# Kernel tuning notes

Hardware: AMD Instinct MI355X
Metric: run time of the kernel (lower is better)

## Reference

```python
import jax, jax.numpy as jnp
import numpy as np

H = 1024   # hidden_size
I = 4096   # intermediate_size
E = 8      # num_local_experts
K = 2      # num_experts_per_tok
B, S = 2, 2048


def setup_inputs() -> dict:
    key = jax.random.key(0)
    ks = jax.random.split(key, 7)
    init = lambda k, shape, fan_in: (jax.random.normal(k, shape, jnp.float32)
                                     / np.float32(np.sqrt(fan_in)))
    return {
        "x": jax.random.normal(ks[0], (B, S, H), jnp.float32),
        "router_gate": init(ks[1], (E, H), H),   # router for gate_proj
        "w_gate": init(ks[2], (E, I, H), H),     # expert weights gate_proj
        "router_up": init(ks[3], (E, H), H),     # router for up_proj
        "w_up": init(ks[4], (E, I, H), H),       # expert weights up_proj
        "router_down": init(ks[5], (E, I), I),   # router for down_proj
        "w_down": init(ks[6], (E, H, I), I),     # expert weights down_proj
    }


def _moe_linear(x, router_w, expert_w):
    """Top-K routed linear. x:[T,din] router_w:[E,din] expert_w:[E,dout,din]."""
    n_exp = router_w.shape[0]
    logits = x @ router_w.T                      # [T, E]
    vals, idx = jax.lax.top_k(logits, K)         # [T, K]
    probs = jax.nn.softmax(vals, axis=-1)        # softmax over selected experts
    onehot = jax.nn.one_hot(idx, n_exp, dtype=x.dtype)    # [T, K, E]
    combine = jnp.einsum('tk,tke->te', probs, onehot)     # [T, E] sparse combine weights
    out = jnp.zeros((x.shape[0], expert_w.shape[1]), x.dtype)
    for e in range(n_exp):  # fixed small expert count
        out = out + combine[:, e:e + 1] * (x @ expert_w[e].T)
    return out


def reference(x, router_gate, w_gate, router_up, w_up, router_down, w_down):
    b, s, h = x.shape
    xt = x.reshape(b * s, h)                     # tokens [T, H]
    g = _moe_linear(xt, router_gate, w_gate)     # [T, I]
    u = _moe_linear(xt, router_up, w_up)         # [T, I]
    inter = jax.nn.silu(g) * u                   # SwiGLU
    d = _moe_linear(inter, router_down, w_down)  # [T, H]
    return d.reshape(b, s, h)
```

## Files before the change

kernel.cpp:

```cpp
#include <hip/hip_runtime.h>
#include <cmath>

typedef float    f32x4 __attribute__((ext_vector_type(4)));
typedef _Float16 f16x8 __attribute__((ext_vector_type(8)));

#define T_NUM 4096
#define H_DIM 1024
#define I_DIM 4096
#define MAXTILES 40

#define M_COUNTS   0
#define M_CURSORS  48
#define M_OFFSETS  96
#define M_NTILES   144
#define M_TILE_E   152
#define M_TILE_M   392
#define M_TOPKI    1024
#define M_TOPKP    25600
#define M_STOK     50176
#define M_SPRB     74752

__device__ __forceinline__ float wave_sum(float v) {
  v += __shfl_xor(v, 32);
  v += __shfl_xor(v, 16);
  v += __shfl_xor(v, 8);
  v += __shfl_xor(v, 4);
  v += __shfl_xor(v, 2);
  v += __shfl_xor(v, 1);
  return v;
}

__device__ __forceinline__ void topk_write(int* meta, int layer, int t, const float* v) {
  int e0 = 0; float v0 = v[0];
  #pragma unroll
  for (int e = 1; e < 8; ++e) { if (v[e] > v0) { v0 = v[e]; e0 = e; } }
  int e1 = 0; float v1 = -3.4e38f;
  #pragma unroll
  for (int e = 0; e < 8; ++e) { if (e != e0 && v[e] > v1) { v1 = v[e]; e1 = e; } }
  float ex = expf(v1 - v0);
  float p0 = 1.f / (1.f + ex);
  float p1 = ex / (1.f + ex);
  meta[M_TOPKI + (layer * T_NUM + t) * 2    ] = e0;
  meta[M_TOPKI + (layer * T_NUM + t) * 2 + 1] = e1;
  ((float*)meta)[M_TOPKP + (layer * T_NUM + t) * 2    ] = p0;
  ((float*)meta)[M_TOPKP + (layer * T_NUM + t) * 2 + 1] = p1;
}

__global__ __launch_bounds__(256) void router_gu(const float* __restrict__ x,
    const float* __restrict__ Rg, const float* __restrict__ Ru, int* __restrict__ meta)
{
  int w = threadIdx.x >> 6, lane = threadIdx.x & 63;
  int t = blockIdx.x * 4 + w;
  const float* xr = x + (size_t)t * H_DIM + lane * 4;
  f32x4 xv[4];
  #pragma unroll
  for (int c = 0; c < 4; ++c) xv[c] = *(const f32x4*)(xr + c * 256);
  float lg[8], lu[8];
  #pragma unroll
  for (int e = 0; e < 8; ++e) {
    const float* rg = Rg + (size_t)e * H_DIM + lane * 4;
    const float* ru = Ru + (size_t)e * H_DIM + lane * 4;
    float sg = 0.f, su = 0.f;
    #pragma unroll
    for (int c = 0; c < 4; ++c) {
      f32x4 a = *(const f32x4*)(rg + c * 256);
      f32x4 b = *(const f32x4*)(ru + c * 256);
      sg += a[0]*xv[c][0] + a[1]*xv[c][1] + a[2]*xv[c][2] + a[3]*xv[c][3];
      su += b[0]*xv[c][0] + b[1]*xv[c][1] + b[2]*xv[c][2] + b[3]*xv[c][3];
    }
    lg[e] = wave_sum(sg);
    lu[e] = wave_sum(su);
  }
  if (lane == 0) {
    topk_write(meta, 0, t, lg);
    topk_write(meta, 1, t, lu);
  }
}

__global__ __launch_bounds__(256) void route_finalize(int* __restrict__ meta, int l0, int nl) {
  __shared__ int cnt_s[32];
  __shared__ int off_s[32];
  __shared__ int cur_s[32];
  int tid = threadIdx.x;
  if (tid < 32) { cnt_s[tid] = 0; cur_s[tid] = 0; }
  __syncthreads();
  for (int t = tid; t < T_NUM; t += 256) {
    for (int l = l0; l < l0 + nl; ++l) {
      int li = l - l0;
      #pragma unroll
      for (int k = 0; k < 2; ++k) {
        int e = meta[M_TOPKI + (l * T_NUM + t) * 2 + k];
        atomicAdd(&cnt_s[li * 16 + k * 8 + e], 1);
      }
    }
  }
  __syncthreads();
  if (tid == 0) {
    for (int l = l0; l < l0 + nl; ++l) {
      int li = l - l0;
      int off = 0;
      for (int k = 0; k < 2; ++k) {
        int nt = 0;
        for (int e = 0; e < 8; ++e) {
          int s = (l * 2 + k) * 8 + e;
          int c = cnt_s[li * 16 + k * 8 + e];
          meta[M_COUNTS + s] = c;
          meta[M_OFFSETS + s] = off;
          off_s[li * 16 + k * 8 + e] = off;
          for (int m = 0; m < c; m += 128) {
            meta[M_TILE_E + (l * 2 + k) * MAXTILES + nt] = e;
            meta[M_TILE_M + (l * 2 + k) * MAXTILES + nt] = m;
            ++nt;
          }
          off += c;
        }
        meta[M_NTILES + l * 2 + k] = nt;
      }
    }
  }
  __syncthreads();
  for (int t = tid; t < T_NUM; t += 256) {
    for (int l = l0; l < l0 + nl; ++l) {
      int li = l - l0;
      #pragma unroll
      for (int k = 0; k < 2; ++k) {
        int e = meta[M_TOPKI + (l * T_NUM + t) * 2 + k];
        float p = ((float*)meta)[M_TOPKP + (l * T_NUM + t) * 2 + k];
        int si = li * 16 + k * 8 + e;
        int pos = off_s[si] + atomicAdd(&cur_s[si], 1);
        meta[M_STOK + l * 8192 + pos] = t;
        ((float*)meta)[M_SPRB + l * 8192 + pos] = p;
      }
    }
  }
}

template<int SPLITS>
__global__ __launch_bounds__(256) void convert_w(const float* __restrict__ W,
    _Float16* __restrict__ Whi, _Float16* __restrict__ Wlo, int NB, int KT)
{
  size_t g = (size_t)blockIdx.x * 256 + threadIdx.x;
  int c   = (int)(g >> 9);
  int rem = (int)(g & 511);
  int fq = rem >> 7, r = rem & 127;
  int e  = c / (NB * KT);
  int nb = (c / KT) % NB;
  int kt = c - (c / KT) * KT;
  int K = KT * 32, N = NB * 128;
  const float* src = W + ((size_t)(e * N + nb * 128 + r)) * K + kt * 32 + fq * 8;
  f32x4 v0 = *(const f32x4*)src;
  f32x4 v1 = *(const f32x4*)(src + 4);
  f16x8 h, l;
  #pragma unroll
  for (int q = 0; q < 8; ++q) {
    float v = (q < 4) ? v0[q] : v1[q - 4];
    _Float16 hv = (_Float16)v;
    h[q] = hv;
    l[q] = (_Float16)(v - (float)hv);
  }
  size_t dst = (size_t)c * 4096 + (size_t)rem * 8;
  *(f16x8*)(Whi + dst) = h;
  if constexpr (SPLITS == 3) *(f16x8*)(Wlo + dst) = l;
}

__global__ __launch_bounds__(256) void gather_a(const float* __restrict__ X,
    _Float16* __restrict__ Apass, const int* __restrict__ meta, int layer, int kk)
{
  int pass = layer * 2 + kk;
  int tile = blockIdx.x >> 5;
  int kt   = blockIdx.x & 31;
  if (tile >= meta[M_NTILES + pass]) return;
  int e    = meta[M_TILE_E + pass * MAXTILES + tile];
  int m0   = meta[M_TILE_M + pass * MAXTILES + tile];
  int sidx = pass * 8 + e;
  int cnt  = meta[M_COUNTS + sidx];
  int seg  = meta[M_OFFSETS + sidx];
  const int* stok = meta + M_STOK + layer * 8192 + seg;
  size_t cb = ((size_t)tile * 32 + kt) * 8192;
  #pragma unroll
  for (int j = 0; j < 2; ++j) {
    int idx = threadIdx.x * 2 + j;
    int fq = idx >> 7, row = idx & 127;
    int m = m0 + row; if (m >= cnt) m = cnt - 1;
    const float* src = X + (size_t)stok[m] * H_DIM + kt * 32 + fq * 8;
    f32x4 v0 = *(const f32x4*)src;
    f32x4 v1 = *(const f32x4*)(src + 4);
    f16x8 h, l;
    #pragma unroll
    for (int q = 0; q < 8; ++q) {
      float v = (q < 4) ? v0[q] : v1[q - 4];
      _Float16 hv = (_Float16)v;
      h[q] = hv;
      l[q] = (_Float16)(v - (float)hv);
    }
    *(f16x8*)(Apass + cb + (size_t)idx * 8) = h;
    *(f16x8*)(Apass + cb + 4096 + (size_t)idx * 8) = l;
  }
}

__global__ __launch_bounds__(256) void gather_d(const float* __restrict__ G,
    _Float16* __restrict__ Ad, const int* __restrict__ meta, int kk)
{
  int pass = 4 + kk;
  int tile = blockIdx.x >> 7;
  int kt   = blockIdx.x & 127;
  if (tile >= meta[M_NTILES + pass]) return;
  int e    = meta[M_TILE_E + pass * MAXTILES + tile];
  int m0   = meta[M_TILE_M + pass * MAXTILES + tile];
  int sidx = pass * 8 + e;
  int cnt  = meta[M_COUNTS + sidx];
  int seg  = meta[M_OFFSETS + sidx];
  const int* stok = meta + M_STOK + 2 * 8192 + seg;
  size_t cb = ((size_t)tile * 128 + kt) * 4096;
  #pragma unroll
  for (int j = 0; j < 2; ++j) {
    int idx = threadIdx.x * 2 + j;
    int fq = idx >> 7, row = idx & 127;
    int m = m0 + row; if (m >= cnt) m = cnt - 1;
    const float* src = G + (size_t)stok[m] * I_DIM + kt * 32 + fq * 8;
    f32x4 v0 = *(const f32x4*)src;
    f32x4 v1 = *(const f32x4*)(src + 4);
    f16x8 h;
    #pragma unroll
    for (int q = 0; q < 8; ++q) h[q] = (_Float16)((q < 4) ? v0[q] : v1[q - 4]);
    *(f16x8*)(Ad + cb + (size_t)idx * 8) = h;
  }
}

__device__ __forceinline__ void gload16(const _Float16* g, _Float16* l) {
  __builtin_amdgcn_global_load_lds(
      (const __attribute__((address_space(1))) void*)g,
      (__attribute__((address_space(3))) void*)l, 16, 0, 0);
}

template<int SPLITS, int ADD, int N, int NB, int STEPS, int SPLITK>
__global__ __launch_bounds__(256, 2) void moe_gemm7(
    const _Float16* __restrict__ Aimg,
    const _Float16* __restrict__ Whi, const _Float16* __restrict__ Wlo,
    float* __restrict__ Out, float* __restrict__ Scr,
    const int* __restrict__ meta, int layer, int kk)
{
  constexpr int NWG = MAXTILES * NB * SPLITK;
  constexpr int Q8  = NWG / 8;
  constexpr int WCH = (SPLITS == 3) ? 1 : 2;

  int orig = (int)blockIdx.x;
  int logical = (orig & 7) * Q8 + (orig >> 3);
  int kc = 0, rem = logical;
  if constexpr (SPLITK == 2) { kc = logical / (MAXTILES * NB); rem = logical - kc * (MAXTILES * NB); }
  int tx = rem / NB;
  int ny = rem - tx * NB;

  int pass = layer * 2 + kk;
  if (tx >= meta[M_NTILES + pass]) return;
  int e    = meta[M_TILE_E + pass * MAXTILES + tx];
  int m0   = meta[M_TILE_M + pass * MAXTILES + tx];
  int sidx = pass * 8 + e;
  int cnt  = meta[M_COUNTS + sidx];
  int seg  = meta[M_OFFSETS + sidx];
  int n0   = ny * 128;

  __shared__ __align__(16) _Float16 sA[3 * 8192];

  int tid = threadIdx.x, lane = tid & 63, w = tid >> 6;
  int wr = w >> 1, wc = w & 1, fr = lane & 15, fq = lane >> 4;

  const int*   stok = meta + M_STOK + layer * 8192 + seg;
  const float* sprb = (const float*)meta + M_SPRB + layer * 8192 + seg;

  const _Float16* At = Aimg + ((size_t)tx * SPLITK + kc) * STEPS * 8192;
  size_t wpanel = (size_t)(e * NB + ny) * (STEPS * WCH * SPLITK) * 4096;
  int kb = kc * STEPS * WCH;
  const _Float16* WhL = Whi + wpanel + (size_t)kb * 4096 + (fq * 128 + wc * 64 + fr) * 8;
  const _Float16* WlL = Wlo + wpanel + (size_t)kb * 4096 + (fq * 128 + wc * 64 + fr) * 8;

  auto stageA = [&](int it, int slot) {
    const _Float16* s0 = At + (size_t)it * 8192 + w * 1024 + lane * 8;
    _Float16* d0 = sA + slot * 8192 + w * 1024;
    gload16(s0,        d0);
    gload16(s0 + 512,  d0 + 512);
    gload16(s0 + 4096, d0 + 4096);
    gload16(s0 + 4608, d0 + 4608);
  };
  auto loadW = [&](int it, f16x8 (&wh)[WCH][4], f16x8 (&wl)[1][4]) {
    #pragma unroll
    for (int c = 0; c < WCH; ++c) {
      size_t cb = (size_t)(it * WCH + c) * 4096;
      #pragma unroll
      for (int ni = 0; ni < 4; ++ni) wh[c][ni] = *(const f16x8*)(WhL + cb + ni * 128);
    }
    if constexpr (SPLITS == 3) {
      size_t cb = (size_t)it * 4096;
      #pragma unroll
      for (int ni = 0; ni < 4; ++ni) wl[0][ni] = *(const f16x8*)(WlL + cb + ni * 128);
    }
  };

  int aoff = (fq * 128 + wr * 64 + fr) * 8;

  f32x4 acc[4][4];
  #pragma unroll
  for (int i = 0; i < 4; ++i)
    #pragma unroll
    for (int j = 0; j < 4; ++j) acc[i][j] = f32x4{0.f, 0.f, 0.f, 0.f};

  f16x8 w0h[WCH][4], w0l[1][4], w1h[WCH][4], w1l[1][4];

  auto step = [&](int it, int rc, int rs,
                  f16x8 (&cwh)[WCH][4], f16x8 (&cwl)[1][4],
                  f16x8 (&nwh)[WCH][4], f16x8 (&nwl)[1][4]) {
    int it2 = (it + 2 < STEPS) ? it + 2 : STEPS - 1;
    int it1 = (it + 1 < STEPS) ? it + 1 : STEPS - 1;
    stageA(it2, rs);
    loadW(it1, nwh, nwl);
    __builtin_amdgcn_sched_barrier(0);

    const _Float16* A0 = sA + rc * 8192;
    __builtin_amdgcn_s_setprio(1);
    if constexpr (SPLITS == 3) {
      f16x8 ah[4], al[4];
      #pragma unroll
      for (int mi = 0; mi < 4; ++mi) ah[mi] = *(const f16x8*)(A0 + aoff + mi * 128);
      #pragma unroll
      for (int mi = 0; mi < 4; ++mi) al[mi] = *(const f16x8*)(A0 + 4096 + aoff + mi * 128);
      #pragma unroll
      for (int mi = 0; mi < 4; ++mi)
        #pragma unroll
        for (int ni = 0; ni < 4; ++ni)
          acc[mi][ni] = __builtin_amdgcn_mfma_f32_16x16x32_f16(ah[mi], cwh[0][ni], acc[mi][ni], 0, 0, 0);
      #pragma unroll
      for (int mi = 0; mi < 4; ++mi)
        #pragma unroll
        for (int ni = 0; ni < 4; ++ni)
          acc[mi][ni] = __builtin_amdgcn_mfma_f32_16x16x32_f16(ah[mi], cwl[0][ni], acc[mi][ni], 0, 0, 0);
      #pragma unroll
      for (int mi = 0; mi < 4; ++mi)
        #pragma unroll
        for (int ni = 0; ni < 4; ++ni)
          acc[mi][ni] = __builtin_amdgcn_mfma_f32_16x16x32_f16(al[mi], cwh[0][ni], acc[mi][ni], 0, 0, 0);
    } else {
      #pragma unroll
      for (int c = 0; c < WCH; ++c) {
        f16x8 ah[4];
        #pragma unroll
        for (int mi = 0; mi < 4; ++mi) ah[mi] = *(const f16x8*)(A0 + c * 4096 + aoff + mi * 128);
        #pragma unroll
        for (int mi = 0; mi < 4; ++mi)
          #pragma unroll
          for (int ni = 0; ni < 4; ++ni)
            acc[mi][ni] = __builtin_amdgcn_mfma_f32_16x16x32_f16(ah[mi], cwh[c][ni], acc[mi][ni], 0, 0, 0);
      }
    }
    __builtin_amdgcn_s_setprio(0);

    __builtin_amdgcn_sched_barrier(0);
    asm volatile("s_waitcnt vmcnt(12)" ::: "memory");
    __builtin_amdgcn_s_barrier();
    __builtin_amdgcn_sched_barrier(0);
  };

  stageA(0, 0);
  stageA(1 < STEPS ? 1 : 0, 1);
  loadW(0, w0h, w0l);
  __builtin_amdgcn_sched_barrier(0);
  asm volatile("s_waitcnt vmcnt(12)" ::: "memory");
  __builtin_amdgcn_s_barrier();
  __builtin_amdgcn_sched_barrier(0);

  int rc = 0, rs = 2;
  for (int it = 0; it < STEPS; it += 2) {
    step(it,     rc, rs, w0h, w0l, w1h, w1l);
    rc = (rc == 2) ? 0 : rc + 1; rs = (rs == 2) ? 0 : rs + 1;
    step(it + 1, rc, rs, w1h, w1l, w0h, w0l);
    rc = (rc == 2) ? 0 : rc + 1; rs = (rs == 2) ? 0 : rs + 1;
  }

  float* dst = (SPLITK == 2 && kc == 1) ? Scr : Out;
  #pragma unroll
  for (int mi = 0; mi < 4; ++mi) {
    #pragma unroll
    for (int jj = 0; jj < 4; ++jj) {
      int lm = wr * 64 + mi * 16 + fq * 4 + jj;
      int gm = m0 + lm;
      if (gm < cnt) {
        int tok = stok[gm];
        float p = sprb[gm];
        float* orow = dst + (size_t)tok * N + n0 + wc * 64 + fr;
        #pragma unroll
        for (int ni = 0; ni < 4; ++ni) {
          float v = p * acc[mi][ni][jj];
          if constexpr (ADD) orow[ni * 16] += v; else orow[ni * 16] = v;
        }
      }
    }
  }
}

__global__ __launch_bounds__(256) void swiglu_router(float* __restrict__ g,
    const float* __restrict__ u, const float* __restrict__ Rd, int* __restrict__ meta)
{
  int t = blockIdx.x, tid = threadIdx.x;
  float part[8];
  #pragma unroll
  for (int e = 0; e < 8; ++e) part[e] = 0.f;
  float* gr = g + (size_t)t * I_DIM;
  const float* ur = u + (size_t)t * I_DIM;
  #pragma unroll
  for (int cc = 0; cc < 4; ++cc) {
    int i = cc * 1024 + tid * 4;
    f32x4 gv = *(const f32x4*)(gr + i);
    f32x4 uv = *(const f32x4*)(ur + i);
    f32x4 iv;
    #pragma unroll
    for (int j = 0; j < 4; ++j) {
      float xx = gv[j];
      iv[j] = (xx / (1.f + expf(-xx))) * uv[j];
    }
    *(f32x4*)(gr + i) = iv;
    #pragma unroll
    for (int e = 0; e < 8; ++e) {
      f32x4 rv = *(const f32x4*)(Rd + (size_t)e * I_DIM + i);
      part[e] += rv[0]*iv[0] + rv[1]*iv[1] + rv[2]*iv[2] + rv[3]*iv[3];
    }
  }
  __shared__ float red[4][8];
  int w = tid >> 6, lane = tid & 63;
  #pragma unroll
  for (int e = 0; e < 8; ++e) {
    float s = wave_sum(part[e]);
    if (lane == 0) red[w][e] = s;
  }
  __syncthreads();
  if (tid == 0) {
    float lg[8];
    #pragma unroll
    for (int e = 0; e < 8; ++e) lg[e] = red[0][e] + red[1][e] + red[2][e] + red[3][e];
    topk_write(meta, 2, t, lg);
  }
}

__global__ __launch_bounds__(256) void combine_kernel(float* __restrict__ out,
                                                      const float* __restrict__ scr)
{
  int i = blockIdx.x * 1024 + threadIdx.x * 4;
  f32x4 a = *(const f32x4*)(out + i);
  f32x4 b = *(const f32x4*)(scr + i);
  #pragma unroll
  for (int j = 0; j < 4; ++j) a[j] += b[j];
  *(f32x4*)(out + i) = a;
}

extern "C" void kernel_launch(void* const* d_in, const int* in_sizes, int n_in,
                              void* d_out, int out_size, void* d_ws, size_t ws_size,
                              hipStream_t stream)
{
  const float* x  = (const float*)d_in[0];
  const float* Rg = (const float*)d_in[1];
  const float* Wg = (const float*)d_in[2];
  const float* Ru = (const float*)d_in[3];
  const float* Wu = (const float*)d_in[4];
  const float* Rd = (const float*)d_in[5];
  const float* Wd = (const float*)d_in[6];
  float* out = (float*)d_out;
  char* ws = (char*)d_ws;

  _Float16* Wth = (_Float16*)ws;
  _Float16* Wtl = (_Float16*)(ws + (size_t)67108864);
  float* g   = (float*)(ws + (size_t)134217728);
  float* u   = (float*)(ws + (size_t)201326592);
  int*  meta = (int*)(ws + (size_t)268435456);
  _Float16* Apass = (_Float16*)(ws + (size_t)269484032);
  _Float16* Ad    = (_Float16*)(ws + (size_t)201326592);
  float* dscr     = (float*)(ws + (size_t)269484032);

  router_gu<<<dim3(T_NUM / 4), 256, 0, stream>>>(x, Rg, Ru, meta);
  route_finalize<<<dim3(1), 256, 0, stream>>>(meta, 0, 2);

  convert_w<3><<<dim3(16384), 256, 0, stream>>>(Wg, Wth, Wtl, 32, 32);
  gather_a<<<dim3(MAXTILES * 32), 256, 0, stream>>>(x, Apass, meta, 0, 0);
  moe_gemm7<3, 0, I_DIM, 32, 32, 1><<<dim3(MAXTILES * 32), 256, 0, stream>>>(
      Apass, Wth, Wtl, g, g, meta, 0, 0);
  gather_a<<<dim3(MAXTILES * 32), 256, 0, stream>>>(x, Apass, meta, 0, 1);
  moe_gemm7<3, 1, I_DIM, 32, 32, 1><<<dim3(MAXTILES * 32), 256, 0, stream>>>(
      Apass, Wth, Wtl, g, g, meta, 0, 1);

  convert_w<3><<<dim3(16384), 256, 0, stream>>>(Wu, Wth, Wtl, 32, 32);
  gather_a<<<dim3(MAXTILES * 32), 256, 0, stream>>>(x, Apass, meta, 1, 0);
  moe_gemm7<3, 0, I_DIM, 32, 32, 1><<<dim3(MAXTILES * 32), 256, 0, stream>>>(
      Apass, Wth, Wtl, u, u, meta, 1, 0);
  gather_a<<<dim3(MAXTILES * 32), 256, 0, stream>>>(x, Apass, meta, 1, 1);
  moe_gemm7<3, 1, I_DIM, 32, 32, 1><<<dim3(MAXTILES * 32), 256, 0, stream>>>(
      Apass, Wth, Wtl, u, u, meta, 1, 1);

  swiglu_router<<<dim3(T_NUM), 256, 0, stream>>>(g, u, Rd, meta);
  route_finalize<<<dim3(1), 256, 0, stream>>>(meta, 2, 1);

  convert_w<1><<<dim3(16384), 256, 0, stream>>>(Wd, Wth, Wth, 8, 128);
  gather_d<<<dim3(MAXTILES * 128), 256, 0, stream>>>(g, Ad, meta, 0);
  moe_gemm7<1, 0, H_DIM, 8, 32, 2><<<dim3(MAXTILES * 8 * 2), 256, 0, stream>>>(
      Ad, Wth, Wth, out, dscr, meta, 2, 0);
  gather_d<<<dim3(MAXTILES * 128), 256, 0, stream>>>(g, Ad, meta, 1);
  moe_gemm7<1, 1, H_DIM, 8, 32, 2><<<dim3(MAXTILES * 8 * 2), 256, 0, stream>>>(
      Ad, Wth, Wth, out, dscr, meta, 2, 1);
  combine_kernel<<<dim3(T_NUM), 256, 0, stream>>>(out, dscr);
}
```

Before: 1.080 ms.

## Deepen weight register prefetch to two steps ahead with triple buffering

The MoE GEMM now keeps three register buffers of weight fragments and issues weight loads two iterations ahead, matching the A-tile LDS staging distance, instead of one. The loop is unrolled by three and the waitcnt threshold rises so more global loads stay in flight. The goal is to hide global-memory latency for the weight stream, at the cost of more VGPRs, which could spill or lower occupancy under the launch bound of 2 blocks per SIMD.

```diff
diff --git a/kernel.cpp b/kernel.cpp
--- a/kernel.cpp
+++ b/kernel.cpp
@@ -234,7 +234,7 @@
 }
 
 template<int SPLITS, int ADD, int N, int NB, int STEPS, int SPLITK>
-__global__ __launch_bounds__(256, 2) void moe_gemm7(
+__global__ __launch_bounds__(256, 2) void moe_gemm8(
     const _Float16* __restrict__ Aimg,
     const _Float16* __restrict__ Whi, const _Float16* __restrict__ Wlo,
     float* __restrict__ Out, float* __restrict__ Scr,
@@ -304,15 +304,16 @@
     #pragma unroll
     for (int j = 0; j < 4; ++j) acc[i][j] = f32x4{0.f, 0.f, 0.f, 0.f};
 
-  f16x8 w0h[WCH][4], w0l[1][4], w1h[WCH][4], w1l[1][4];
-
-  auto step = [&](int it, int rc, int rs,
-                  f16x8 (&cwh)[WCH][4], f16x8 (&cwl)[1][4],
-                  f16x8 (&nwh)[WCH][4], f16x8 (&nwl)[1][4]) {
+  f16x8 wAh[WCH][4], wAl[1][4], wBh[WCH][4], wBl[1][4], wCh[WCH][4], wCl[1][4];
+
+  int rc = 0, rs = 2;
+
+  auto step = [&](int it, f16x8 (&cwh)[WCH][4], f16x8 (&cwl)[1][4],
+                          f16x8 (&nwh)[WCH][4], f16x8 (&nwl)[1][4]) {
     int it2 = (it + 2 < STEPS) ? it + 2 : STEPS - 1;
-    int it1 = (it + 1 < STEPS) ? it + 1 : STEPS - 1;
     stageA(it2, rs);
-    loadW(it1, nwh, nwl);
+    __builtin_amdgcn_sched_barrier(0);
+    loadW(it2, nwh, nwl);
     __builtin_amdgcn_sched_barrier(0);
 
     const _Float16* A0 = sA + rc * 8192;
@@ -354,26 +355,33 @@
     __builtin_amdgcn_s_setprio(0);
 
     __builtin_amdgcn_sched_barrier(0);
-    asm volatile("s_waitcnt vmcnt(12)" ::: "memory");
+    asm volatile("s_waitcnt vmcnt(20)" ::: "memory");
     __builtin_amdgcn_s_barrier();
     __builtin_amdgcn_sched_barrier(0);
+    rc = (rc == 2) ? 0 : rc + 1;
+    rs = (rs == 2) ? 0 : rs + 1;
   };
 
   stageA(0, 0);
+  __builtin_amdgcn_sched_barrier(0);
   stageA(1 < STEPS ? 1 : 0, 1);
-  loadW(0, w0h, w0l);
   __builtin_amdgcn_sched_barrier(0);
-  asm volatile("s_waitcnt vmcnt(12)" ::: "memory");
+  loadW(0, wAh, wAl);
+  __builtin_amdgcn_sched_barrier(0);
+  loadW(1 < STEPS ? 1 : 0, wBh, wBl);
+  __builtin_amdgcn_sched_barrier(0);
+  asm volatile("s_waitcnt vmcnt(20)" ::: "memory");
   __builtin_amdgcn_s_barrier();
   __builtin_amdgcn_sched_barrier(0);
 
-  int rc = 0, rs = 2;
-  for (int it = 0; it < STEPS; it += 2) {
-    step(it,     rc, rs, w0h, w0l, w1h, w1l);
-    rc = (rc == 2) ? 0 : rc + 1; rs = (rs == 2) ? 0 : rs + 1;
-    step(it + 1, rc, rs, w1h, w1l, w0h, w0l);
-    rc = (rc == 2) ? 0 : rc + 1; rs = (rs == 2) ? 0 : rs + 1;
-  }
+  int it = 0;
+  for (; it + 3 <= STEPS; it += 3) {
+    step(it,     wAh, wAl, wCh, wCl);
+    step(it + 1, wBh, wBl, wAh, wAl);
+    step(it + 2, wCh, wCl, wBh, wBl);
+  }
+  if (it < STEPS) { step(it, wAh, wAl, wCh, wCl); ++it; }
+  if (it < STEPS) { step(it, wBh, wBl, wCh, wCl); }
 
   float* dst = (SPLITK == 2 && kc == 1) ? Scr : Out;
   #pragma unroll
@@ -478,18 +486,18 @@
 
   convert_w<3><<<dim3(16384), 256, 0, stream>>>(Wg, Wth, Wtl, 32, 32);
   gather_a<<<dim3(MAXTILES * 32), 256, 0, stream>>>(x, Apass, meta, 0, 0);
-  moe_gemm7<3, 0, I_DIM, 32, 32, 1><<<dim3(MAXTILES * 32), 256, 0, stream>>>(
+  moe_gemm8<3, 0, I_DIM, 32, 32, 1><<<dim3(MAXTILES * 32), 256, 0, stream>>>(
       Apass, Wth, Wtl, g, g, meta, 0, 0);
   gather_a<<<dim3(MAXTILES * 32), 256, 0, stream>>>(x, Apass, meta, 0, 1);
-  moe_gemm7<3, 1, I_DIM, 32, 32, 1><<<dim3(MAXTILES * 32), 256, 0, stream>>>(
+  moe_gemm8<3, 1, I_DIM, 32, 32, 1><<<dim3(MAXTILES * 32), 256, 0, stream>>>(
       Apass, Wth, Wtl, g, g, meta, 0, 1);
 
   convert_w<3><<<dim3(16384), 256, 0, stream>>>(Wu, Wth, Wtl, 32, 32);
   gather_a<<<dim3(MAXTILES * 32), 256, 0, stream>>>(x, Apass, meta, 1, 0);
-  moe_gemm7<3, 0, I_DIM, 32, 32, 1><<<dim3(MAXTILES * 32), 256, 0, stream>>>(
+  moe_gemm8<3, 0, I_DIM, 32, 32, 1><<<dim3(MAXTILES * 32), 256, 0, stream>>>(
       Apass, Wth, Wtl, u, u, meta, 1, 0);
   gather_a<<<dim3(MAXTILES * 32), 256, 0, stream>>>(x, Apass, meta, 1, 1);
-  moe_gemm7<3, 1, I_DIM, 32, 32, 1><<<dim3(MAXTILES * 32), 256, 0, stream>>>(
+  moe_gemm8<3, 1, I_DIM, 32, 32, 1><<<dim3(MAXTILES * 32), 256, 0, stream>>>(
       Apass, Wth, Wtl, u, u, meta, 1, 1);
 
   swiglu_router<<<dim3(T_NUM), 256, 0, stream>>>(g, u, Rd, meta);
@@ -497,10 +505,10 @@
 
   convert_w<1><<<dim3(16384), 256, 0, stream>>>(Wd, Wth, Wth, 8, 128);
   gather_d<<<dim3(MAXTILES * 128), 256, 0, stream>>>(g, Ad, meta, 0);
-  moe_gemm7<1, 0, H_DIM, 8, 32, 2><<<dim3(MAXTILES * 8 * 2), 256, 0, stream>>>(
+  moe_gemm8<1, 0, H_DIM, 8, 32, 2><<<dim3(MAXTILES * 8 * 2), 256, 0, stream>>>(
       Ad, Wth, Wth, out, dscr, meta, 2, 0);
   gather_d<<<dim3(MAXTILES * 128), 256, 0, stream>>>(g, Ad, meta, 1);
-  moe_gemm7<1, 1, H_DIM, 8, 32, 2><<<dim3(MAXTILES * 8 * 2), 256, 0, stream>>>(
+  moe_gemm8<1, 1, H_DIM, 8, 32, 2><<<dim3(MAXTILES * 8 * 2), 256, 0, stream>>>(
       Ad, Wth, Wth, out, dscr, meta, 2, 1);
   combine_kernel<<<dim3(T_NUM), 256, 0, stream>>>(out, dscr);
 }
```

Result: slower. 1.124 ms (+4.1%).

## Make MoE GEMM persistent with XCD-strided tile loop and higher occupancy

Applied to the files above, without the earlier changes.

The grouped GEMM kernel becomes a persistent kernel launched with a fixed grid of 768 blocks. Each block loops over logical tiles assigned to its XCD slot and skips empty tiles cheaply, instead of launching one block per possible tile and exiting early. Launch bounds go from 2 to 3 blocks per CU, which raises occupancy but tightens the register budget. A full vmcnt wait plus a barrier between tiles keeps the shared-memory ring safe, at the cost of draining the pipeline at each tile boundary.

```diff
diff --git a/kernel.cpp b/kernel.cpp
--- a/kernel.cpp
+++ b/kernel.cpp
@@ -234,7 +234,7 @@
 }
 
 template<int SPLITS, int ADD, int N, int NB, int STEPS, int SPLITK>
-__global__ __launch_bounds__(256, 2) void moe_gemm7(
+__global__ __launch_bounds__(256, 3) void moe_gemm9(
     const _Float16* __restrict__ Aimg,
     const _Float16* __restrict__ Whi, const _Float16* __restrict__ Wlo,
     float* __restrict__ Out, float* __restrict__ Scr,
@@ -244,152 +244,158 @@
   constexpr int Q8  = NWG / 8;
   constexpr int WCH = (SPLITS == 3) ? 1 : 2;
 
-  int orig = (int)blockIdx.x;
-  int logical = (orig & 7) * Q8 + (orig >> 3);
-  int kc = 0, rem = logical;
-  if constexpr (SPLITK == 2) { kc = logical / (MAXTILES * NB); rem = logical - kc * (MAXTILES * NB); }
-  int tx = rem / NB;
-  int ny = rem - tx * NB;
-
+  int xcd  = (int)blockIdx.x & 7;
+  int slot = (int)blockIdx.x >> 3;
+  int nper = (int)gridDim.x >> 3;
   int pass = layer * 2 + kk;
-  if (tx >= meta[M_NTILES + pass]) return;
-  int e    = meta[M_TILE_E + pass * MAXTILES + tx];
-  int m0   = meta[M_TILE_M + pass * MAXTILES + tx];
-  int sidx = pass * 8 + e;
-  int cnt  = meta[M_COUNTS + sidx];
-  int seg  = meta[M_OFFSETS + sidx];
-  int n0   = ny * 128;
+  int ntiles = meta[M_NTILES + pass];
 
   __shared__ __align__(16) _Float16 sA[3 * 8192];
 
   int tid = threadIdx.x, lane = tid & 63, w = tid >> 6;
   int wr = w >> 1, wc = w & 1, fr = lane & 15, fq = lane >> 4;
-
-  const int*   stok = meta + M_STOK + layer * 8192 + seg;
-  const float* sprb = (const float*)meta + M_SPRB + layer * 8192 + seg;
-
-  const _Float16* At = Aimg + ((size_t)tx * SPLITK + kc) * STEPS * 8192;
-  size_t wpanel = (size_t)(e * NB + ny) * (STEPS * WCH * SPLITK) * 4096;
-  int kb = kc * STEPS * WCH;
-  const _Float16* WhL = Whi + wpanel + (size_t)kb * 4096 + (fq * 128 + wc * 64 + fr) * 8;
-  const _Float16* WlL = Wlo + wpanel + (size_t)kb * 4096 + (fq * 128 + wc * 64 + fr) * 8;
-
-  auto stageA = [&](int it, int slot) {
-    const _Float16* s0 = At + (size_t)it * 8192 + w * 1024 + lane * 8;
-    _Float16* d0 = sA + slot * 8192 + w * 1024;
-    gload16(s0,        d0);
-    gload16(s0 + 512,  d0 + 512);
-    gload16(s0 + 4096, d0 + 4096);
-    gload16(s0 + 4608, d0 + 4608);
-  };
-  auto loadW = [&](int it, f16x8 (&wh)[WCH][4], f16x8 (&wl)[1][4]) {
-    #pragma unroll
-    for (int c = 0; c < WCH; ++c) {
-      size_t cb = (size_t)(it * WCH + c) * 4096;
-      #pragma unroll
-      for (int ni = 0; ni < 4; ++ni) wh[c][ni] = *(const f16x8*)(WhL + cb + ni * 128);
-    }
-    if constexpr (SPLITS == 3) {
-      size_t cb = (size_t)it * 4096;
-      #pragma unroll
-      for (int ni = 0; ni < 4; ++ni) wl[0][ni] = *(const f16x8*)(WlL + cb + ni * 128);
-    }
-  };
-
   int aoff = (fq * 128 + wr * 64 + fr) * 8;
 
-  f32x4 acc[4][4];
-  #pragma unroll
-  for (int i = 0; i < 4; ++i)
-    #pragma unroll
-    for (int j = 0; j < 4; ++j) acc[i][j] = f32x4{0.f, 0.f, 0.f, 0.f};
-
-  f16x8 w0h[WCH][4], w0l[1][4], w1h[WCH][4], w1l[1][4];
-
-  auto step = [&](int it, int rc, int rs,
-                  f16x8 (&cwh)[WCH][4], f16x8 (&cwl)[1][4],
-                  f16x8 (&nwh)[WCH][4], f16x8 (&nwl)[1][4]) {
-    int it2 = (it + 2 < STEPS) ? it + 2 : STEPS - 1;
-    int it1 = (it + 1 < STEPS) ? it + 1 : STEPS - 1;
-    stageA(it2, rs);
-    loadW(it1, nwh, nwl);
-    __builtin_amdgcn_sched_barrier(0);
-
-    const _Float16* A0 = sA + rc * 8192;
-    __builtin_amdgcn_s_setprio(1);
-    if constexpr (SPLITS == 3) {
-      f16x8 ah[4], al[4];
-      #pragma unroll
-      for (int mi = 0; mi < 4; ++mi) ah[mi] = *(const f16x8*)(A0 + aoff + mi * 128);
-      #pragma unroll
-      for (int mi = 0; mi < 4; ++mi) al[mi] = *(const f16x8*)(A0 + 4096 + aoff + mi * 128);
-      #pragma unroll
-      for (int mi = 0; mi < 4; ++mi)
-        #pragma unroll
-        for (int ni = 0; ni < 4; ++ni)
-          acc[mi][ni] = __builtin_amdgcn_mfma_f32_16x16x32_f16(ah[mi], cwh[0][ni], acc[mi][ni], 0, 0, 0);
-      #pragma unroll
-      for (int mi = 0; mi < 4; ++mi)
-        #pragma unroll
-        for (int ni = 0; ni < 4; ++ni)
-          acc[mi][ni] = __builtin_amdgcn_mfma_f32_16x16x32_f16(ah[mi], cwl[0][ni], acc[mi][ni], 0, 0, 0);
-      #pragma unroll
-      for (int mi = 0; mi < 4; ++mi)
-        #pragma unroll
-        for (int ni = 0; ni < 4; ++ni)
-          acc[mi][ni] = __builtin_amdgcn_mfma_f32_16x16x32_f16(al[mi], cwh[0][ni], acc[mi][ni], 0, 0, 0);
-    } else {
+  for (int base = slot; base < Q8; base += nper) {
+    int logical = xcd * Q8 + base;
+    int kc = 0, rem = logical;
+    if constexpr (SPLITK == 2) { kc = logical / (MAXTILES * NB); rem = logical - kc * (MAXTILES * NB); }
+    int tx = rem / NB;
+    int ny = rem - tx * NB;
+    if (tx >= ntiles) continue;
+
+    int e    = meta[M_TILE_E + pass * MAXTILES + tx];
+    int m0   = meta[M_TILE_M + pass * MAXTILES + tx];
+    int sidx = pass * 8 + e;
+    int cnt  = meta[M_COUNTS + sidx];
+    int seg  = meta[M_OFFSETS + sidx];
+    int n0   = ny * 128;
+
+    const int*   stok = meta + M_STOK + layer * 8192 + seg;
+    const float* sprb = (const float*)meta + M_SPRB + layer * 8192 + seg;
+
+    const _Float16* At = Aimg + ((size_t)tx * SPLITK + kc) * STEPS * 8192;
+    size_t wpanel = (size_t)(e * NB + ny) * (STEPS * WCH * SPLITK) * 4096;
+    int kb = kc * STEPS * WCH;
+    const _Float16* WhL = Whi + wpanel + (size_t)kb * 4096 + (fq * 128 + wc * 64 + fr) * 8;
+    const _Float16* WlL = Wlo + wpanel + (size_t)kb * 4096 + (fq * 128 + wc * 64 + fr) * 8;
+
+    auto stageA = [&](int it, int slot2) {
+      const _Float16* s0 = At + (size_t)it * 8192 + w * 1024 + lane * 8;
+      _Float16* d0 = sA + slot2 * 8192 + w * 1024;
+      gload16(s0,        d0);
+      gload16(s0 + 512,  d0 + 512);
+      gload16(s0 + 4096, d0 + 4096);
+      gload16(s0 + 4608, d0 + 4608);
+    };
+    auto loadW = [&](int it, f16x8 (&wh)[WCH][4], f16x8 (&wl)[1][4]) {
       #pragma unroll
       for (int c = 0; c < WCH; ++c) {
-        f16x8 ah[4];
-        #pragma unroll
-        for (int mi = 0; mi < 4; ++mi) ah[mi] = *(const f16x8*)(A0 + c * 4096 + aoff + mi * 128);
+        size_t cb = (size_t)(it * WCH + c) * 4096;
+        #pragma unroll
+        for (int ni = 0; ni < 4; ++ni) wh[c][ni] = *(const f16x8*)(WhL + cb + ni * 128);
+      }
+      if constexpr (SPLITS == 3) {
+        size_t cb = (size_t)it * 4096;
+        #pragma unroll
+        for (int ni = 0; ni < 4; ++ni) wl[0][ni] = *(const f16x8*)(WlL + cb + ni * 128);
+      }
+    };
+
+    f32x4 acc[4][4];
+    #pragma unroll
+    for (int i = 0; i < 4; ++i)
+      #pragma unroll
+      for (int j = 0; j < 4; ++j) acc[i][j] = f32x4{0.f, 0.f, 0.f, 0.f};
+
+    f16x8 w0h[WCH][4], w0l[1][4], w1h[WCH][4], w1l[1][4];
+    int rc = 0, rs = 2;
+
+    auto step = [&](int it, f16x8 (&cwh)[WCH][4], f16x8 (&cwl)[1][4],
+                    f16x8 (&nwh)[WCH][4], f16x8 (&nwl)[1][4]) {
+      int it2 = (it + 2 < STEPS) ? it + 2 : STEPS - 1;
+      int it1 = (it + 1 < STEPS) ? it + 1 : STEPS - 1;
+      stageA(it2, rs);
+      loadW(it1, nwh, nwl);
+      __builtin_amdgcn_sched_barrier(0);
+
+      const _Float16* A0 = sA + rc * 8192;
+      __builtin_amdgcn_s_setprio(1);
+      if constexpr (SPLITS == 3) {
+        f16x8 ah[4], al[4];
+        #pragma unroll
+        for (int mi = 0; mi < 4; ++mi) ah[mi] = *(const f16x8*)(A0 + aoff + mi * 128);
+        #pragma unroll
+        for (int mi = 0; mi < 4; ++mi) al[mi] = *(const f16x8*)(A0 + 4096 + aoff + mi * 128);
         #pragma unroll
         for (int mi = 0; mi < 4; ++mi)
           #pragma unroll
           for (int ni = 0; ni < 4; ++ni)
-            acc[mi][ni] = __builtin_amdgcn_mfma_f32_16x16x32_f16(ah[mi], cwh[c][ni], acc[mi][ni], 0, 0, 0);
-      }
-    }
-    __builtin_amdgcn_s_setprio(0);
-
+            acc[mi][ni] = __builtin_amdgcn_mfma_f32_16x16x32_f16(ah[mi], cwh[0][ni], acc[mi][ni], 0, 0, 0);
+        #pragma unroll
+        for (int mi = 0; mi < 4; ++mi)
+          #pragma unroll
+          for (int ni = 0; ni < 4; ++ni)
+            acc[mi][ni] = __builtin_amdgcn_mfma_f32_16x16x32_f16(ah[mi], cwl[0][ni], acc[mi][ni], 0, 0, 0);
+        #pragma unroll
+        for (int mi = 0; mi < 4; ++mi)
+          #pragma unroll
+          for (int ni = 0; ni < 4; ++ni)
+            acc[mi][ni] = __builtin_amdgcn_mfma_f32_16x16x32_f16(al[mi], cwh[0][ni], acc[mi][ni], 0, 0, 0);
+      } else {
+        #pragma unroll
+        for (int c = 0; c < WCH; ++c) {
+          f16x8 ah[4];
+          #pragma unroll
+          for (int mi = 0; mi < 4; ++mi) ah[mi] = *(const f16x8*)(A0 + c * 4096 + aoff + mi * 128);
+          #pragma unroll
+          for (int mi = 0; mi < 4; ++mi)
+            #pragma unroll
+            for (int ni = 0; ni < 4; ++ni)
+              acc[mi][ni] = __builtin_amdgcn_mfma_f32_16x16x32_f16(ah[mi], cwh[c][ni], acc[mi][ni], 0, 0, 0);
+        }
+      }
+      __builtin_amdgcn_s_setprio(0);
+
+      __builtin_amdgcn_sched_barrier(0);
+      asm volatile("s_waitcnt vmcnt(12)" ::: "memory");
+      __builtin_amdgcn_s_barrier();
+      __builtin_amdgcn_sched_barrier(0);
+      rc = (rc == 2) ? 0 : rc + 1;
+      rs = (rs == 2) ? 0 : rs + 1;
+    };
+
+    asm volatile("s_waitcnt vmcnt(0)" ::: "memory");
+    __builtin_amdgcn_s_barrier();
+    stageA(0, 0);
+    stageA(1 < STEPS ? 1 : 0, 1);
+    loadW(0, w0h, w0l);
     __builtin_amdgcn_sched_barrier(0);
     asm volatile("s_waitcnt vmcnt(12)" ::: "memory");
     __builtin_amdgcn_s_barrier();
     __builtin_amdgcn_sched_barrier(0);
-  };
-
-  stageA(0, 0);
-  stageA(1 < STEPS ? 1 : 0, 1);
-  loadW(0, w0h, w0l);
-  __builtin_amdgcn_sched_barrier(0);
-  asm volatile("s_waitcnt vmcnt(12)" ::: "memory");
-  __builtin_amdgcn_s_barrier();
-  __builtin_amdgcn_sched_barrier(0);
-
-  int rc = 0, rs = 2;
-  for (int it = 0; it < STEPS; it += 2) {
-    step(it,     rc, rs, w0h, w0l, w1h, w1l);
-    rc = (rc == 2) ? 0 : rc + 1; rs = (rs == 2) ? 0 : rs + 1;
-    step(it + 1, rc, rs, w1h, w1l, w0h, w0l);
-    rc = (rc == 2) ? 0 : rc + 1; rs = (rs == 2) ? 0 : rs + 1;
-  }
-
-  float* dst = (SPLITK == 2 && kc == 1) ? Scr : Out;
-  #pragma unroll
-  for (int mi = 0; mi < 4; ++mi) {
-    #pragma unroll
-    for (int jj = 0; jj < 4; ++jj) {
-      int lm = wr * 64 + mi * 16 + fq * 4 + jj;
-      int gm = m0 + lm;
-      if (gm < cnt) {
-        int tok = stok[gm];
-        float p = sprb[gm];
-        float* orow = dst + (size_t)tok * N + n0 + wc * 64 + fr;
-        #pragma unroll
-        for (int ni = 0; ni < 4; ++ni) {
-          float v = p * acc[mi][ni][jj];
-          if constexpr (ADD) orow[ni * 16] += v; else orow[ni * 16] = v;
+
+    for (int it = 0; it < STEPS; it += 2) {
+      step(it,     w0h, w0l, w1h, w1l);
+      step(it + 1, w1h, w1l, w0h, w0l);
+    }
+
+    float* dst = (SPLITK == 2 && kc == 1) ? Scr : Out;
+    #pragma unroll
+    for (int mi = 0; mi < 4; ++mi) {
+      #pragma unroll
+      for (int jj = 0; jj < 4; ++jj) {
+        int lm = wr * 64 + mi * 16 + fq * 4 + jj;
+        int gm = m0 + lm;
+        if (gm < cnt) {
+          int tok = stok[gm];
+          float p = sprb[gm];
+          float* orow = dst + (size_t)tok * N + n0 + wc * 64 + fr;
+          #pragma unroll
+          for (int ni = 0; ni < 4; ++ni) {
+            float v = p * acc[mi][ni][jj];
+            if constexpr (ADD) orow[ni * 16] += v; else orow[ni * 16] = v;
+          }
         }
       }
     }
@@ -478,18 +484,18 @@
 
   convert_w<3><<<dim3(16384), 256, 0, stream>>>(Wg, Wth, Wtl, 32, 32);
   gather_a<<<dim3(MAXTILES * 32), 256, 0, stream>>>(x, Apass, meta, 0, 0);
-  moe_gemm7<3, 0, I_DIM, 32, 32, 1><<<dim3(MAXTILES * 32), 256, 0, stream>>>(
+  moe_gemm9<3, 0, I_DIM, 32, 32, 1><<<dim3(768), 256, 0, stream>>>(
       Apass, Wth, Wtl, g, g, meta, 0, 0);
   gather_a<<<dim3(MAXTILES * 32), 256, 0, stream>>>(x, Apass, meta, 0, 1);
-  moe_gemm7<3, 1, I_DIM, 32, 32, 1><<<dim3(MAXTILES * 32), 256, 0, stream>>>(
+  moe_gemm9<3, 1, I_DIM, 32, 32, 1><<<dim3(768), 256, 0, stream>>>(
       Apass, Wth, Wtl, g, g, meta, 0, 1);
 
   convert_w<3><<<dim3(16384), 256, 0, stream>>>(Wu, Wth, Wtl, 32, 32);
   gather_a<<<dim3(MAXTILES * 32), 256, 0, stream>>>(x, Apass, meta, 1, 0);
-  moe_gemm7<3, 0, I_DIM, 32, 32, 1><<<dim3(MAXTILES * 32), 256, 0, stream>>>(
+  moe_gemm9<3, 0, I_DIM, 32, 32, 1><<<dim3(768), 256, 0, stream>>>(
       Apass, Wth, Wtl, u, u, meta, 1, 0);
   gather_a<<<dim3(MAXTILES * 32), 256, 0, stream>>>(x, Apass, meta, 1, 1);
-  moe_gemm7<3, 1, I_DIM, 32, 32, 1><<<dim3(MAXTILES * 32), 256, 0, stream>>>(
+  moe_gemm9<3, 1, I_DIM, 32, 32, 1><<<dim3(768), 256, 0, stream>>>(
       Apass, Wth, Wtl, u, u, meta, 1, 1);
 
   swiglu_router<<<dim3(T_NUM), 256, 0, stream>>>(g, u, Rd, meta);
@@ -497,10 +503,10 @@
 
   convert_w<1><<<dim3(16384), 256, 0, stream>>>(Wd, Wth, Wth, 8, 128);
   gather_d<<<dim3(MAXTILES * 128), 256, 0, stream>>>(g, Ad, meta, 0);
-  moe_gemm7<1, 0, H_DIM, 8, 32, 2><<<dim3(MAXTILES * 8 * 2), 256, 0, stream>>>(
+  moe_gemm9<1, 0, H_DIM, 8, 32, 2><<<dim3(768), 256, 0, stream>>>(
       Ad, Wth, Wth, out, dscr, meta, 2, 0);
   gather_d<<<dim3(MAXTILES * 128), 256, 0, stream>>>(g, Ad, meta, 1);
-  moe_gemm7<1, 1, H_DIM, 8, 32, 2><<<dim3(MAXTILES * 8 * 2), 256, 0, stream>>>(
+  moe_gemm9<1, 1, H_DIM, 8, 32, 2><<<dim3(768), 256, 0, stream>>>(
       Ad, Wth, Wth, out, dscr, meta, 2, 1);
   combine_kernel<<<dim3(T_NUM), 256, 0, stream>>>(out, dscr);
 }
```

New measurement: 1.075 ms. No clear change (-0.5%).

## Load A fragments directly from global into registers, dropping LDS staging

Applied to the files above, without the earlier changes.

The grouped GEMM no longer stages the A tile in a triple-buffered shared-memory ring via global_load_lds with barriers. Each wave now reads its A fragments straight from global memory into registers, double-buffered alongside the weight fragments. This removes LDS traffic, the LDS allocation and the per-step barriers. The trade-off is that the two column-waves each fetch the same A rows redundantly from global or L2, and register pressure rises under the two-waves-per-SIMD launch bound.

```diff
diff --git a/kernel.cpp b/kernel.cpp
--- a/kernel.cpp
+++ b/kernel.cpp
@@ -227,14 +227,8 @@
   }
 }
 
-__device__ __forceinline__ void gload16(const _Float16* g, _Float16* l) {
-  __builtin_amdgcn_global_load_lds(
-      (const __attribute__((address_space(1))) void*)g,
-      (__attribute__((address_space(3))) void*)l, 16, 0, 0);
-}
-
 template<int SPLITS, int ADD, int N, int NB, int STEPS, int SPLITK>
-__global__ __launch_bounds__(256, 2) void moe_gemm7(
+__global__ __launch_bounds__(256, 2) void moe_gemm12(
     const _Float16* __restrict__ Aimg,
     const _Float16* __restrict__ Whi, const _Float16* __restrict__ Wlo,
     float* __restrict__ Out, float* __restrict__ Scr,
@@ -260,27 +254,25 @@
   int seg  = meta[M_OFFSETS + sidx];
   int n0   = ny * 128;
 
-  __shared__ __align__(16) _Float16 sA[3 * 8192];
-
   int tid = threadIdx.x, lane = tid & 63, w = tid >> 6;
   int wr = w >> 1, wc = w & 1, fr = lane & 15, fq = lane >> 4;
 
   const int*   stok = meta + M_STOK + layer * 8192 + seg;
   const float* sprb = (const float*)meta + M_SPRB + layer * 8192 + seg;
 
-  const _Float16* At = Aimg + ((size_t)tx * SPLITK + kc) * STEPS * 8192;
+  const _Float16* AtL = Aimg + ((size_t)tx * SPLITK + kc) * STEPS * 8192
+                      + (fq * 128 + wr * 64 + fr) * 8;
   size_t wpanel = (size_t)(e * NB + ny) * (STEPS * WCH * SPLITK) * 4096;
   int kb = kc * STEPS * WCH;
   const _Float16* WhL = Whi + wpanel + (size_t)kb * 4096 + (fq * 128 + wc * 64 + fr) * 8;
   const _Float16* WlL = Wlo + wpanel + (size_t)kb * 4096 + (fq * 128 + wc * 64 + fr) * 8;
 
-  auto stageA = [&](int it, int slot) {
-    const _Float16* s0 = At + (size_t)it * 8192 + w * 1024 + lane * 8;
-    _Float16* d0 = sA + slot * 8192 + w * 1024;
-    gload16(s0,        d0);
-    gload16(s0 + 512,  d0 + 512);
-    gload16(s0 + 4096, d0 + 4096);
-    gload16(s0 + 4608, d0 + 4608);
+  auto loadA = [&](int it, f16x8 (&a0)[4], f16x8 (&a1)[4]) {
+    const _Float16* s = AtL + (size_t)it * 8192;
+    #pragma unroll
+    for (int mi = 0; mi < 4; ++mi) a0[mi] = *(const f16x8*)(s + mi * 128);
+    #pragma unroll
+    for (int mi = 0; mi < 4; ++mi) a1[mi] = *(const f16x8*)(s + 4096 + mi * 128);
   };
   auto loadW = [&](int it, f16x8 (&wh)[WCH][4], f16x8 (&wl)[1][4]) {
     #pragma unroll
@@ -296,83 +288,60 @@
     }
   };
 
-  int aoff = (fq * 128 + wr * 64 + fr) * 8;
-
   f32x4 acc[4][4];
   #pragma unroll
   for (int i = 0; i < 4; ++i)
     #pragma unroll
     for (int j = 0; j < 4; ++j) acc[i][j] = f32x4{0.f, 0.f, 0.f, 0.f};
 
-  f16x8 w0h[WCH][4], w0l[1][4], w1h[WCH][4], w1l[1][4];
-
-  auto step = [&](int it, int rc, int rs,
-                  f16x8 (&cwh)[WCH][4], f16x8 (&cwl)[1][4],
-                  f16x8 (&nwh)[WCH][4], f16x8 (&nwl)[1][4]) {
-    int it2 = (it + 2 < STEPS) ? it + 2 : STEPS - 1;
-    int it1 = (it + 1 < STEPS) ? it + 1 : STEPS - 1;
-    stageA(it2, rs);
-    loadW(it1, nwh, nwl);
-    __builtin_amdgcn_sched_barrier(0);
-
-    const _Float16* A0 = sA + rc * 8192;
+  auto mfma_step = [&](f16x8 (&a0)[4], f16x8 (&a1)[4],
+                       f16x8 (&wh)[WCH][4], f16x8 (&wl)[1][4]) {
     __builtin_amdgcn_s_setprio(1);
     if constexpr (SPLITS == 3) {
-      f16x8 ah[4], al[4];
-      #pragma unroll
-      for (int mi = 0; mi < 4; ++mi) ah[mi] = *(const f16x8*)(A0 + aoff + mi * 128);
-      #pragma unroll
-      for (int mi = 0; mi < 4; ++mi) al[mi] = *(const f16x8*)(A0 + 4096 + aoff + mi * 128);
       #pragma unroll
       for (int mi = 0; mi < 4; ++mi)
         #pragma unroll
         for (int ni = 0; ni < 4; ++ni)
-          acc[mi][ni] = __builtin_amdgcn_mfma_f32_16x16x32_f16(ah[mi], cwh[0][ni], acc[mi][ni], 0, 0, 0);
+          acc[mi][ni] = __builtin_amdgcn_mfma_f32_16x16x32_f16(a0[mi], wh[0][ni], acc[mi][ni], 0, 0, 0);
       #pragma unroll
       for (int mi = 0; mi < 4; ++mi)
         #pragma unroll
         for (int ni = 0; ni < 4; ++ni)
-          acc[mi][ni] = __builtin_amdgcn_mfma_f32_16x16x32_f16(ah[mi], cwl[0][ni], acc[mi][ni], 0, 0, 0);
+          acc[mi][ni] = __builtin_amdgcn_mfma_f32_16x16x32_f16(a0[mi], wl[0][ni], acc[mi][ni], 0, 0, 0);
       #pragma unroll
       for (int mi = 0; mi < 4; ++mi)
         #pragma unroll
         for (int ni = 0; ni < 4; ++ni)
-          acc[mi][ni] = __builtin_amdgcn_mfma_f32_16x16x32_f16(al[mi], cwh[0][ni], acc[mi][ni], 0, 0, 0);
+          acc[mi][ni] = __builtin_amdgcn_mfma_f32_16x16x32_f16(a1[mi], wh[0][ni], acc[mi][ni], 0, 0, 0);
     } else {
       #pragma unroll
-      for (int c = 0; c < WCH; ++c) {
-        f16x8 ah[4];
-        #pragma unroll
-        for (int mi = 0; mi < 4; ++mi) ah[mi] = *(const f16x8*)(A0 + c * 4096 + aoff + mi * 128);
-        #pragma unroll
-        for (int mi = 0; mi < 4; ++mi)
-          #pragma unroll
-          for (int ni = 0; ni < 4; ++ni)
-            acc[mi][ni] = __builtin_amdgcn_mfma_f32_16x16x32_f16(ah[mi], cwh[c][ni], acc[mi][ni], 0, 0, 0);
-      }
+      for (int mi = 0; mi < 4; ++mi)
+        #pragma unroll
+        for (int ni = 0; ni < 4; ++ni)
+          acc[mi][ni] = __builtin_amdgcn_mfma_f32_16x16x32_f16(a0[mi], wh[0][ni], acc[mi][ni], 0, 0, 0);
+      #pragma unroll
+      for (int mi = 0; mi < 4; ++mi)
+        #pragma unroll
+        for (int ni = 0; ni < 4; ++ni)
+          acc[mi][ni] = __builtin_amdgcn_mfma_f32_16x16x32_f16(a1[mi], wh[1][ni], acc[mi][ni], 0, 0, 0);
     }
     __builtin_amdgcn_s_setprio(0);
-
-    __builtin_amdgcn_sched_barrier(0);
-    asm volatile("s_waitcnt vmcnt(12)" ::: "memory");
-    __builtin_amdgcn_s_barrier();
-    __builtin_amdgcn_sched_barrier(0);
   };
 
-  stageA(0, 0);
-  stageA(1 < STEPS ? 1 : 0, 1);
-  loadW(0, w0h, w0l);
-  __builtin_amdgcn_sched_barrier(0);
-  asm volatile("s_waitcnt vmcnt(12)" ::: "memory");
-  __builtin_amdgcn_s_barrier();
-  __builtin_amdgcn_sched_barrier(0);
-
-  int rc = 0, rs = 2;
+  f16x8 a0A[4], a1A[4], a0B[4], a1B[4];
+  f16x8 wHA[WCH][4], wLA[1][4], wHB[WCH][4], wLB[1][4];
+
+  loadA(0, a0A, a1A);
+  loadW(0, wHA, wLA);
   for (int it = 0; it < STEPS; it += 2) {
-    step(it,     rc, rs, w0h, w0l, w1h, w1l);
-    rc = (rc == 2) ? 0 : rc + 1; rs = (rs == 2) ? 0 : rs + 1;
-    step(it + 1, rc, rs, w1h, w1l, w0h, w0l);
-    rc = (rc == 2) ? 0 : rc + 1; rs = (rs == 2) ? 0 : rs + 1;
+    int it1 = (it + 1 < STEPS) ? it + 1 : it;
+    int it2 = (it + 2 < STEPS) ? it + 2 : it1;
+    loadA(it1, a0B, a1B);
+    loadW(it1, wHB, wLB);
+    mfma_step(a0A, a1A, wHA, wLA);
+    loadA(it2, a0A, a1A);
+    loadW(it2, wHA, wLA);
+    mfma_step(a0B, a1B, wHB, wLB);
   }
 
   float* dst = (SPLITK == 2 && kc == 1) ? Scr : Out;
@@ -478,18 +447,18 @@
 
   convert_w<3><<<dim3(16384), 256, 0, stream>>>(Wg, Wth, Wtl, 32, 32);
   gather_a<<<dim3(MAXTILES * 32), 256, 0, stream>>>(x, Apass, meta, 0, 0);
-  moe_gemm7<3, 0, I_DIM, 32, 32, 1><<<dim3(MAXTILES * 32), 256, 0, stream>>>(
+  moe_gemm12<3, 0, I_DIM, 32, 32, 1><<<dim3(MAXTILES * 32), 256, 0, stream>>>(
       Apass, Wth, Wtl, g, g, meta, 0, 0);
   gather_a<<<dim3(MAXTILES * 32), 256, 0, stream>>>(x, Apass, meta, 0, 1);
-  moe_gemm7<3, 1, I_DIM, 32, 32, 1><<<dim3(MAXTILES * 32), 256, 0, stream>>>(
+  moe_gemm12<3, 1, I_DIM, 32, 32, 1><<<dim3(MAXTILES * 32), 256, 0, stream>>>(
       Apass, Wth, Wtl, g, g, meta, 0, 1);
 
   convert_w<3><<<dim3(16384), 256, 0, stream>>>(Wu, Wth, Wtl, 32, 32);
   gather_a<<<dim3(MAXTILES * 32), 256, 0, stream>>>(x, Apass, meta, 1, 0);
-  moe_gemm7<3, 0, I_DIM, 32, 32, 1><<<dim3(MAXTILES * 32), 256, 0, stream>>>(
+  moe_gemm12<3, 0, I_DIM, 32, 32, 1><<<dim3(MAXTILES * 32), 256, 0, stream>>>(
       Apass, Wth, Wtl, u, u, meta, 1, 0);
   gather_a<<<dim3(MAXTILES * 32), 256, 0, stream>>>(x, Apass, meta, 1, 1);
-  moe_gemm7<3, 1, I_DIM, 32, 32, 1><<<dim3(MAXTILES * 32), 256, 0, stream>>>(
+  moe_gemm12<3, 1, I_DIM, 32, 32, 1><<<dim3(MAXTILES * 32), 256, 0, stream>>>(
       Apass, Wth, Wtl, u, u, meta, 1, 1);
 
   swiglu_router<<<dim3(T_NUM), 256, 0, stream>>>(g, u, Rd, meta);
@@ -497,10 +466,10 @@
 
   convert_w<1><<<dim3(16384), 256, 0, stream>>>(Wd, Wth, Wth, 8, 128);
   gather_d<<<dim3(MAXTILES * 128), 256, 0, stream>>>(g, Ad, meta, 0);
-  moe_gemm7<1, 0, H_DIM, 8, 32, 2><<<dim3(MAXTILES * 8 * 2), 256, 0, stream>>>(
+  moe_gemm12<1, 0, H_DIM, 8, 32, 2><<<dim3(MAXTILES * 8 * 2), 256, 0, stream>>>(
       Ad, Wth, Wth, out, dscr, meta, 2, 0);
   gather_d<<<dim3(MAXTILES * 128), 256, 0, stream>>>(g, Ad, meta, 1);
-  moe_gemm7<1, 1, H_DIM, 8, 32, 2><<<dim3(MAXTILES * 8 * 2), 256, 0, stream>>>(
+  moe_gemm12<1, 1, H_DIM, 8, 32, 2><<<dim3(MAXTILES * 8 * 2), 256, 0, stream>>>(
       Ad, Wth, Wth, out, dscr, meta, 2, 1);
   combine_kernel<<<dim3(T_NUM), 256, 0, stream>>>(out, dscr);
 }
```

After: 1.129 ms. 4.5% more time.
